# Performance work log

Hardware: AMD Instinct MI355X
Metric: run time of the kernel (lower is better)

## Reference

```python
import jax, jax.numpy as jnp
import numpy as np

T, B, D_IN, D_H = 1024, 64, 256, 256


def setup_inputs() -> dict:
    key = jax.random.key(0)
    ks = jax.random.split(key, 9)
    s = 1.0 / np.sqrt(D_IN + D_H)  # torch Linear default init scale
    def lin(k):
        kw, kb = jax.random.split(k)
        W = jax.random.uniform(kw, (D_H, D_IN + D_H), minval=-s, maxval=s, dtype=jnp.float32)
        b = jax.random.uniform(kb, (D_H,), minval=-s, maxval=s, dtype=jnp.float32)
        return W, b
    W_f, b_f = lin(ks[0])
    W_i, b_i = lin(ks[1])
    W_g, b_g = lin(ks[2])
    W_o, b_o = lin(ks[3])
    inputs = jax.random.normal(ks[4], (T, B, D_IN), dtype=jnp.float32)
    h0 = jnp.zeros((B, D_H), dtype=jnp.float32)
    c0 = jnp.zeros((B, D_H), dtype=jnp.float32)
    return {"inputs": inputs, "h0": h0, "c0": c0,
            "W_f": W_f, "b_f": b_f, "W_i": W_i, "b_i": b_i,
            "W_g": W_g, "b_g": b_g, "W_o": W_o, "b_o": b_o}


def reference(inputs, h0, c0, W_f, b_f, W_i, b_i, W_g, b_g, W_o, b_o):
    # Fuse the 4 gate GEMMs into one: stack weights -> [4H, D_in+H]
    W = jnp.concatenate([W_f, W_i, W_g, W_o], axis=0)      # [4H, D]
    b = jnp.concatenate([b_f, b_i, b_g, b_o], axis=0)      # [4H]
    H = h0.shape[-1]

    def step(carry, x):
        h, c = carry
        combined = jnp.concatenate([x, h], axis=1)          # [B, D_in+H]
        gates = combined @ W.T + b                          # [B, 4H]
        f = jax.nn.sigmoid(gates[:, 0 * H:1 * H])
        i = jax.nn.sigmoid(gates[:, 1 * H:2 * H])
        g = jnp.tanh(gates[:, 2 * H:3 * H])
        o = jax.nn.sigmoid(gates[:, 3 * H:4 * H])
        c_new = f * c + i * g
        h_new = o * jnp.tanh(c_new)
        return (h_new, c_new), h_new

    (h, c), outputs = jax.lax.scan(step, (h0, c0), inputs)
    return outputs, h, c
```

## Files before the change

kernel.cpp:

```cpp
#include <hip/hip_runtime.h>
#include <cstdint>
#include <cstddef>

#define T_STEPS 1024
#define NB 64
#define DIN 256
#define DH 256
#define DW 512
#define G4 1024

typedef _Float16 h2 __attribute__((ext_vector_type(2)));
typedef _Float16 h4 __attribute__((ext_vector_type(4)));
typedef _Float16 h8 __attribute__((ext_vector_type(8)));
typedef float f4 __attribute__((ext_vector_type(4)));
typedef float f32x4 __attribute__((ext_vector_type(4)));
typedef int i4v __attribute__((ext_vector_type(4)));

static __device__ __forceinline__ float rcp_(float x) {
#if __has_builtin(__builtin_amdgcn_rcpf)
  return __builtin_amdgcn_rcpf(x);
#else
  return 1.0f / x;
#endif
}

static __device__ __forceinline__ float sigmoid_(float x) {
  return rcp_(1.f + __expf(-x));
}
static __device__ __forceinline__ float tanh_(float x) {
  float e = __expf(2.f * x);
  return 1.f - 2.f * rcp_(e + 1.f);
}

static __device__ __forceinline__ int sdot4_(int a, int b, int c) {
#if __has_builtin(__builtin_amdgcn_sdot4)
  return __builtin_amdgcn_sdot4(a, b, c, false);
#else
  int r = c;
#pragma unroll
  for (int k = 0; k < 4; ++k)
    r += (int)(signed char)(a >> (8 * k)) * (int)(signed char)(b >> (8 * k));
  return r;
#endif
}

static __device__ __forceinline__ float dpp_swap1(float x) {
  int r = __builtin_amdgcn_update_dpp(0, __builtin_bit_cast(int, x),
                                      0xB1, 0xF, 0xF, true);
  return __builtin_bit_cast(float, r);
}

__global__ void kconv_w(const float* __restrict__ Wf, const float* __restrict__ Wi,
                        const float* __restrict__ Wg, const float* __restrict__ Wo,
                        h2* __restrict__ wxfs) {
  int kp = blockIdx.x >> 2;
  int gate = blockIdx.x & 3;
  int j = threadIdx.x;
  const float* W = gate == 0 ? Wf : gate == 1 ? Wi : gate == 2 ? Wg : Wo;
  const float* row = W + (size_t)j * DW;
  h2 v; v[0] = (_Float16)row[2*kp]; v[1] = (_Float16)row[2*kp + 1];
  int ks = kp >> 4, lg = (kp >> 2) & 3, slot = kp & 3;
  int nt = j >> 4, li = j & 15;
  size_t h8idx = (((size_t)gate * 8 + ks) * 16 + nt) * 64 + lg * 16 + li;
  wxfs[h8idx * 4 + slot] = v;
}

__global__ void kscale(const float* __restrict__ Wf, const float* __restrict__ Wi,
                       const float* __restrict__ Wg, const float* __restrict__ Wo,
                       signed char* __restrict__ wq, float* __restrict__ cs) {
  int gate = blockIdx.x;
  int j = threadIdx.x;
  const float* W = gate == 0 ? Wf : gate == 1 ? Wi : gate == 2 ? Wg : Wo;
  const float* row = W + (size_t)j * DW + DIN;
  float amax = 1e-8f;
#pragma unroll 4
  for (int k4 = 0; k4 < 64; ++k4) {
    f4 v = *(const f4*)(row + 4 * k4);
    amax = fmaxf(amax, fmaxf(fmaxf(fabsf(v[0]), fabsf(v[1])),
                             fmaxf(fabsf(v[2]), fabsf(v[3]))));
  }
  int gr = gate * 256 + j;
  cs[gr] = amax / (127.f * 127.f);
  float inv = 127.f / amax;
  signed char* dst = wq + (size_t)gr * 256;
#pragma unroll 4
  for (int k4 = 0; k4 < 64; ++k4) {
    f4 v = *(const f4*)(row + 4 * k4);
#pragma unroll
    for (int u = 0; u < 4; ++u)
      dst[4 * k4 + u] = (signed char)__float2int_rn(v[u] * inv);
  }
}

__launch_bounds__(256, 2)
__global__ void kxgemm(const float* __restrict__ x,
                       const h8* __restrict__ wxfs,
                       const float* __restrict__ bf, const float* __restrict__ bi,
                       const float* __restrict__ bg, const float* __restrict__ bo,
                       _Float16* __restrict__ Xg,
                       int t0) {
  __shared__ char pool[65536];
  h8 (*xsf)[8][64] = (h8(*)[8][64])pool;
  h8 (*bs)[1024] = (h8(*)[1024])(pool + 32768);

  int tid = threadIdx.x;
  int l = tid & 63;
  int w = tid >> 6;
  int li = l & 15, lg = l >> 4;
  int tl = blockIdx.x >> 2;
  int nb = blockIdx.x & 3;
  int m0 = w * 16;

#pragma unroll
  for (int i = 0; i < 8; ++i) {
    int hi = tid + 256 * i;
    int sw  = hi >> 9;
    int sks = (hi >> 6) & 7;
    int sl  = hi & 63;
    int sli = sl & 15, slg = sl >> 4;
    const float* src = x + ((size_t)(t0 + tl) * NB + sw * 16 + sli) * DIN
                     + sks * 32 + slg * 8;
    f4 a0 = *(const f4*)src;
    f4 a1 = *(const f4*)(src + 4);
    h8 a;
    a[0] = (_Float16)a0[0]; a[1] = (_Float16)a0[1];
    a[2] = (_Float16)a0[2]; a[3] = (_Float16)a0[3];
    a[4] = (_Float16)a1[0]; a[5] = (_Float16)a1[1];
    a[6] = (_Float16)a1[2]; a[7] = (_Float16)a1[3];
    xsf[sw][sks][sl] = a;
  }
  {
    const h8* wsrc = wxfs + (size_t)(nb * 8 + 0) * 1024;
#pragma unroll
    for (int i = 0; i < 4; ++i) bs[0][tid + 256 * i] = wsrc[tid + 256 * i];
  }
  __syncthreads();

  f32x4 acc[16];
#pragma unroll
  for (int nt = 0; nt < 16; ++nt) {
    acc[nt][0] = 0.f; acc[nt][1] = 0.f; acc[nt][2] = 0.f; acc[nt][3] = 0.f;
  }

  for (int ks = 0; ks < 8; ++ks) {
    int buf = ks & 1;
    h8 ld0, ld1, ld2, ld3;
    if (ks < 7) {
      const h8* wn = wxfs + (size_t)(nb * 8 + ks + 1) * 1024;
      ld0 = wn[tid]; ld1 = wn[tid + 256]; ld2 = wn[tid + 512]; ld3 = wn[tid + 768];
    }
    h8 a = xsf[w][ks][l];
#pragma unroll
    for (int nt = 0; nt < 16; ++nt) {
      h8 bb = bs[buf][nt * 64 + l];
      acc[nt] = __builtin_amdgcn_mfma_f32_16x16x32_f16(a, bb, acc[nt], 0, 0, 0);
    }
    if (ks < 7) {
      h8* bt = bs[buf ^ 1];
      bt[tid] = ld0; bt[tid + 256] = ld1; bt[tid + 512] = ld2; bt[tid + 768] = ld3;
    }
    __syncthreads();
  }

  _Float16* osw = (_Float16*)(pool + (size_t)w * 8448);
  const float* biasp = nb == 0 ? bf : nb == 1 ? bi : nb == 2 ? bg : bo;
#pragma unroll
  for (int nt = 0; nt < 16; ++nt) {
    float bv = biasp[nt * 16 + li];
#pragma unroll
    for (int r = 0; r < 4; ++r)
      osw[(lg * 4 + r) * 264 + nt * 16 + li] = (_Float16)(acc[nt][r] + bv);
  }
  _Float16* og = Xg + (size_t)tl * 65536 + (size_t)m0 * 1024 + nb * 256;
#pragma unroll
  for (int it = 0; it < 8; ++it) {
    int i = l + 64 * it;
    int row = i >> 5, c8 = i & 31;
    h8 v = *(const h8*)(const void*)&osw[row * 264 + c8 * 8];
    *(h8*)(void*)(og + (size_t)row * 1024 + c8 * 8) = v;
  }
}

#define CH8(M) M(0) M(1) M(2) M(3) M(4) M(5) M(6) M(7)
#define HB 144

__global__ __launch_bounds__(512, 1)
void klstm(const signed char* __restrict__ wq, const float* __restrict__ cs,
           const _Float16* __restrict__ Xg,
           const float* __restrict__ hsrc, const float* __restrict__ csrc,
           float* __restrict__ out,
           float* __restrict__ hN, float* __restrict__ cN,
           int t0, int Tc) {
  __shared__ __align__(16) char hpool[2][43008];

  int tid = threadIdx.x;
  int b = blockIdx.x;
  int p = tid & 1;
  int j = tid >> 1;

  const i4v* rF = (const i4v*)(wq + ((size_t)(0 * DH + j) * 256) + p * 128);
  const i4v* rI = (const i4v*)(wq + ((size_t)(1 * DH + j) * 256) + p * 128);
  const i4v* rG = (const i4v*)(wq + ((size_t)(2 * DH + j) * 256) + p * 128);
  const i4v* rO = (const i4v*)(wq + ((size_t)(3 * DH + j) * 256) + p * 128);

#define DECLW(c) i4v QF_##c, QI_##c, QG_##c, QO_##c;
  CH8(DECLW)
#undef DECLW
#define LOADW(c) \
  QF_##c = rF[c]; QI_##c = rI[c]; QG_##c = rG[c]; QO_##c = rO[c];
  CH8(LOADW)
#undef LOADW
#define PINW(c) \
  asm volatile("" : "+v"(QF_##c)); asm volatile("" : "+v"(QI_##c)); \
  asm volatile("" : "+v"(QG_##c)); asm volatile("" : "+v"(QO_##c));
  CH8(PINW)
#undef PINW

  float cF = cs[0 * DH + j];
  float cI = cs[1 * DH + j];
  float cG = cs[2 * DH + j];
  float cO = cs[3 * DH + j];

  float creg = csrc[(size_t)b * DH + j];
  if (tid < 256) {
    int pos = (tid < 128) ? tid : (HB + tid - 128);
    float hv = hsrc[(size_t)b * DH + tid];
    hpool[0][pos] = (char)__float2int_rn(fminf(fmaxf(hv, -1.f), 1.f) * 127.f);
  }
  __syncthreads();

  const size_t xstep = (size_t)NB * G4;
  const _Float16* xpA = Xg + (size_t)b * G4 + p * 512 + j;
  const _Float16* xpB = xpA + 256;
  float xA = (float)xpA[0], xB = (float)xpB[0];
  float hlast = 0.f;

  for (int t = 0; t < Tc; ++t) {
    float xAn = 0.f, xBn = 0.f;
    if (t + 1 < Tc) {
      xAn = (float)xpA[(size_t)(t + 1) * xstep];
      xBn = (float)xpB[(size_t)(t + 1) * xstep];
    }
    const char* hb = hpool[t & 1] + p * HB;

    int aF = 0, aI = 0, aG = 0, aO = 0;
#define DOTC(c) { \
    i4v hv = *(const i4v*)(const void*)(hb + 16 * (c)); \
    aF = sdot4_(QF_##c[0], hv[0], aF); aF = sdot4_(QF_##c[1], hv[1], aF); \
    aF = sdot4_(QF_##c[2], hv[2], aF); aF = sdot4_(QF_##c[3], hv[3], aF); \
    aI = sdot4_(QI_##c[0], hv[0], aI); aI = sdot4_(QI_##c[1], hv[1], aI); \
    aI = sdot4_(QI_##c[2], hv[2], aI); aI = sdot4_(QI_##c[3], hv[3], aI); \
    aG = sdot4_(QG_##c[0], hv[0], aG); aG = sdot4_(QG_##c[1], hv[1], aG); \
    aG = sdot4_(QG_##c[2], hv[2], aG); aG = sdot4_(QG_##c[3], hv[3], aG); \
    aO = sdot4_(QO_##c[0], hv[0], aO); aO = sdot4_(QO_##c[1], hv[1], aO); \
    aO = sdot4_(QO_##c[2], hv[2], aO); aO = sdot4_(QO_##c[3], hv[3], aO); }
    CH8(DOTC)
#undef DOTC

    float vF = cF * (float)aF + (p ? 0.f : xA);
    float vI = cI * (float)aI + (p ? 0.f : xB);
    float vG = cG * (float)aG + (p ? xA : 0.f);
    float vO = cO * (float)aO + (p ? xB : 0.f);
    vF += dpp_swap1(vF);
    vI += dpp_swap1(vI);
    vG += dpp_swap1(vG);
    vO += dpp_swap1(vO);

    float f_ = sigmoid_(vF);
    float i_ = sigmoid_(vI);
    float g_ = tanh_(vG);
    float o_ = sigmoid_(vO);

    creg = f_ * creg + i_ * g_;
    float hn = o_ * tanh_(creg);
    hlast = hn;
    if (p == 0) {
      out[((size_t)(t0 + t) * NB + b) * DH + j] = hn;
    } else {
      int pos = (j < 128) ? j : (HB + j - 128);
      hpool[(t + 1) & 1][pos] = (char)__float2int_rn(hn * 127.f);
    }
    __syncthreads();
    xA = xAn; xB = xBn;
  }

  if (p == 0) {
    hN[(size_t)b * DH + j] = hlast;
    cN[(size_t)b * DH + j] = creg;
  }
}

extern "C" void kernel_launch(void* const* d_in, const int* in_sizes, int n_in,
                              void* d_out, int out_size, void* d_ws, size_t ws_size,
                              hipStream_t stream) {
  if (n_in < 11) return;
  const float* x  = (const float*)d_in[0];
  const float* h0 = (const float*)d_in[1];
  const float* c0 = (const float*)d_in[2];
  const float* Wf = (const float*)d_in[3];
  const float* bf = (const float*)d_in[4];
  const float* Wi = (const float*)d_in[5];
  const float* bi = (const float*)d_in[6];
  const float* Wg = (const float*)d_in[7];
  const float* bg = (const float*)d_in[8];
  const float* Wo = (const float*)d_in[9];
  const float* bo = (const float*)d_in[10];

  float* out = (float*)d_out;
  float* hN = out + (size_t)T_STEPS * NB * DH;
  float* cN = hN + (size_t)NB * DH;

  const size_t wxfBytes = (size_t)G4 * 128 * sizeof(h2);
  const size_t wqBytes  = (size_t)G4 * 256;
  const size_t csBytes  = (size_t)G4 * sizeof(float);
  const size_t fixedBytes = wxfBytes + wqBytes + csBytes;
  size_t avail = (ws_size > fixedBytes + 512) ? ws_size - fixedBytes - 512 : 0;
  const size_t perT = (size_t)NB * G4 * 2;
  int Tc = (int)(avail / perT);
  if (Tc > T_STEPS) Tc = T_STEPS;
  if (Tc < 1) Tc = 1;

  _Float16* Xg = (_Float16*)d_ws;
  size_t xgBytes = ((size_t)Tc * perT + 255) / 256 * 256;
  h2* wxfs = (h2*)((char*)d_ws + xgBytes);
  signed char* wq = (signed char*)((char*)d_ws + xgBytes + wxfBytes);
  float* cs = (float*)((char*)d_ws + xgBytes + wxfBytes + wqBytes);

  kconv_w<<<dim3(512), dim3(256), 0, stream>>>(Wf, Wi, Wg, Wo, wxfs);
  kscale<<<dim3(4), dim3(256), 0, stream>>>(Wf, Wi, Wg, Wo, wq, cs);

  for (int t0 = 0; t0 < T_STEPS; t0 += Tc) {
    int tc = (T_STEPS - t0 < Tc) ? (T_STEPS - t0) : Tc;
    kxgemm<<<dim3(tc * 4), dim3(256), 0, stream>>>(x, (const h8*)wxfs,
                                                   bf, bi, bg, bo, Xg, t0);
    const float* hs = (t0 == 0) ? h0 : hN;
    const float* cs_ = (t0 == 0) ? c0 : cN;
    klstm<<<dim3(NB), dim3(512), 0, stream>>>(wq, cs, Xg, hs, cs_,
                                              out, hN, cN, t0, tc);
  }
}
```

Measured before the change: 1.244 ms.

## Process two batch rows per block in LSTM recurrence, halving grid size

Each klstm block now handles two batch elements, reusing the register-resident int8 weights for both hidden vectors and interleaving the two dot-product chains for more ILP. The grid drops from 64 to 32 blocks, and the shared-memory buffer shrinks from a large pool to a small double buffer. Output stores are deferred by one step so they overlap with the next step's compute. Fewer blocks means fewer CUs in use and about twice the per-step work in each block, which could lengthen the serial critical path.

```diff
diff --git a/kernel.cpp b/kernel.cpp
--- a/kernel.cpp
+++ b/kernel.cpp
@@ -183,6 +183,7 @@
 
 #define CH8(M) M(0) M(1) M(2) M(3) M(4) M(5) M(6) M(7)
 #define HB 144
+#define BB 288
 
 __global__ __launch_bounds__(512, 1)
 void klstm(const signed char* __restrict__ wq, const float* __restrict__ cs,
@@ -191,10 +192,11 @@
            float* __restrict__ out,
            float* __restrict__ hN, float* __restrict__ cN,
            int t0, int Tc) {
-  __shared__ __align__(16) char hpool[2][43008];
+  __shared__ __align__(16) char hp[2][2 * BB];
 
   int tid = threadIdx.x;
-  int b = blockIdx.x;
+  int b0 = blockIdx.x * 2;
+  int b1 = b0 + 1;
   int p = tid & 1;
   int j = tid >> 1;
 
@@ -221,72 +223,109 @@
   float cG = cs[2 * DH + j];
   float cO = cs[3 * DH + j];
 
-  float creg = csrc[(size_t)b * DH + j];
-  if (tid < 256) {
-    int pos = (tid < 128) ? tid : (HB + tid - 128);
-    float hv = hsrc[(size_t)b * DH + tid];
-    hpool[0][pos] = (char)__float2int_rn(fminf(fmaxf(hv, -1.f), 1.f) * 127.f);
+  float creg0 = csrc[(size_t)b0 * DH + j];
+  float creg1 = csrc[(size_t)b1 * DH + j];
+
+  {
+    int bt = tid >> 8, e = tid & 255;
+    int pos = (e < 128) ? e : (HB + e - 128);
+    float hv = hsrc[(size_t)(b0 + bt) * DH + e];
+    hp[0][bt * BB + pos] = (char)__float2int_rn(fminf(fmaxf(hv, -1.f), 1.f) * 127.f);
   }
   __syncthreads();
 
   const size_t xstep = (size_t)NB * G4;
-  const _Float16* xpA = Xg + (size_t)b * G4 + p * 512 + j;
-  const _Float16* xpB = xpA + 256;
-  float xA = (float)xpA[0], xB = (float)xpB[0];
-  float hlast = 0.f;
+  const _Float16* xA0p = Xg + (size_t)b0 * G4 + p * 512 + j;
+  const _Float16* xB0p = xA0p + 256;
+  const _Float16* xA1p = Xg + (size_t)b1 * G4 + p * 512 + j;
+  const _Float16* xB1p = xA1p + 256;
+  float xA0 = (float)xA0p[0], xB0 = (float)xB0p[0];
+  float xA1 = (float)xA1p[0], xB1 = (float)xB1p[0];
+  float hp0 = 0.f, hp1 = 0.f;
+  float hl0 = 0.f, hl1 = 0.f;
+
+  float* ob0 = out + (size_t)b0 * DH + j;
+  float* ob1 = out + (size_t)b1 * DH + j;
 
   for (int t = 0; t < Tc; ++t) {
-    float xAn = 0.f, xBn = 0.f;
+    if (p == 0 && t > 0) {
+      ob0[(size_t)(t0 + t - 1) * NB * DH] = hp0;
+      ob1[(size_t)(t0 + t - 1) * NB * DH] = hp1;
+    }
+    float xA0n = 0.f, xB0n = 0.f, xA1n = 0.f, xB1n = 0.f;
     if (t + 1 < Tc) {
-      xAn = (float)xpA[(size_t)(t + 1) * xstep];
-      xBn = (float)xpB[(size_t)(t + 1) * xstep];
-    }
-    const char* hb = hpool[t & 1] + p * HB;
-
-    int aF = 0, aI = 0, aG = 0, aO = 0;
+      size_t o = (size_t)(t + 1) * xstep;
+      xA0n = (float)xA0p[o]; xB0n = (float)xB0p[o];
+      xA1n = (float)xA1p[o]; xB1n = (float)xB1p[o];
+    }
+    const char* hbA = hp[t & 1] + p * HB;
+    const char* hbB = hp[t & 1] + BB + p * HB;
+
+    int aF0 = 0, aI0 = 0, aG0 = 0, aO0 = 0;
+    int aF1 = 0, aI1 = 0, aG1 = 0, aO1 = 0;
 #define DOTC(c) { \
-    i4v hv = *(const i4v*)(const void*)(hb + 16 * (c)); \
-    aF = sdot4_(QF_##c[0], hv[0], aF); aF = sdot4_(QF_##c[1], hv[1], aF); \
-    aF = sdot4_(QF_##c[2], hv[2], aF); aF = sdot4_(QF_##c[3], hv[3], aF); \
-    aI = sdot4_(QI_##c[0], hv[0], aI); aI = sdot4_(QI_##c[1], hv[1], aI); \
-    aI = sdot4_(QI_##c[2], hv[2], aI); aI = sdot4_(QI_##c[3], hv[3], aI); \
-    aG = sdot4_(QG_##c[0], hv[0], aG); aG = sdot4_(QG_##c[1], hv[1], aG); \
-    aG = sdot4_(QG_##c[2], hv[2], aG); aG = sdot4_(QG_##c[3], hv[3], aG); \
-    aO = sdot4_(QO_##c[0], hv[0], aO); aO = sdot4_(QO_##c[1], hv[1], aO); \
-    aO = sdot4_(QO_##c[2], hv[2], aO); aO = sdot4_(QO_##c[3], hv[3], aO); }
+    i4v hA = *(const i4v*)(const void*)(hbA + 16 * (c)); \
+    i4v hB = *(const i4v*)(const void*)(hbB + 16 * (c)); \
+    aF0 = sdot4_(QF_##c[0], hA[0], aF0); aF1 = sdot4_(QF_##c[0], hB[0], aF1); \
+    aF0 = sdot4_(QF_##c[1], hA[1], aF0); aF1 = sdot4_(QF_##c[1], hB[1], aF1); \
+    aF0 = sdot4_(QF_##c[2], hA[2], aF0); aF1 = sdot4_(QF_##c[2], hB[2], aF1); \
+    aF0 = sdot4_(QF_##c[3], hA[3], aF0); aF1 = sdot4_(QF_##c[3], hB[3], aF1); \
+    aI0 = sdot4_(QI_##c[0], hA[0], aI0); aI1 = sdot4_(QI_##c[0], hB[0], aI1); \
+    aI0 = sdot4_(QI_##c[1], hA[1], aI0); aI1 = sdot4_(QI_##c[1], hB[1], aI1); \
+    aI0 = sdot4_(QI_##c[2], hA[2], aI0); aI1 = sdot4_(QI_##c[2], hB[2], aI1); \
+    aI0 = sdot4_(QI_##c[3], hA[3], aI0); aI1 = sdot4_(QI_##c[3], hB[3], aI1); \
+    aG0 = sdot4_(QG_##c[0], hA[0], aG0); aG1 = sdot4_(QG_##c[0], hB[0], aG1); \
+    aG0 = sdot4_(QG_##c[1], hA[1], aG0); aG1 = sdot4_(QG_##c[1], hB[1], aG1); \
+    aG0 = sdot4_(QG_##c[2], hA[2], aG0); aG1 = sdot4_(QG_##c[2], hB[2], aG1); \
+    aG0 = sdot4_(QG_##c[3], hA[3], aG0); aG1 = sdot4_(QG_##c[3], hB[3], aG1); \
+    aO0 = sdot4_(QO_##c[0], hA[0], aO0); aO1 = sdot4_(QO_##c[0], hB[0], aO1); \
+    aO0 = sdot4_(QO_##c[1], hA[1], aO0); aO1 = sdot4_(QO_##c[1], hB[1], aO1); \
+    aO0 = sdot4_(QO_##c[2], hA[2], aO0); aO1 = sdot4_(QO_##c[2], hB[2], aO1); \
+    aO0 = sdot4_(QO_##c[3], hA[3], aO0); aO1 = sdot4_(QO_##c[3], hB[3], aO1); }
     CH8(DOTC)
 #undef DOTC
 
-    float vF = cF * (float)aF + (p ? 0.f : xA);
-    float vI = cI * (float)aI + (p ? 0.f : xB);
-    float vG = cG * (float)aG + (p ? xA : 0.f);
-    float vO = cO * (float)aO + (p ? xB : 0.f);
-    vF += dpp_swap1(vF);
-    vI += dpp_swap1(vI);
-    vG += dpp_swap1(vG);
-    vO += dpp_swap1(vO);
-
-    float f_ = sigmoid_(vF);
-    float i_ = sigmoid_(vI);
-    float g_ = tanh_(vG);
-    float o_ = sigmoid_(vO);
-
-    creg = f_ * creg + i_ * g_;
-    float hn = o_ * tanh_(creg);
-    hlast = hn;
-    if (p == 0) {
-      out[((size_t)(t0 + t) * NB + b) * DH + j] = hn;
-    } else {
+    float vF0 = cF * (float)aF0 + (p ? 0.f : xA0);
+    float vI0 = cI * (float)aI0 + (p ? 0.f : xB0);
+    float vG0 = cG * (float)aG0 + (p ? xA0 : 0.f);
+    float vO0 = cO * (float)aO0 + (p ? xB0 : 0.f);
+    float vF1 = cF * (float)aF1 + (p ? 0.f : xA1);
+    float vI1 = cI * (float)aI1 + (p ? 0.f : xB1);
+    float vG1 = cG * (float)aG1 + (p ? xA1 : 0.f);
+    float vO1 = cO * (float)aO1 + (p ? xB1 : 0.f);
+    vF0 += dpp_swap1(vF0); vF1 += dpp_swap1(vF1);
+    vI0 += dpp_swap1(vI0); vI1 += dpp_swap1(vI1);
+    vG0 += dpp_swap1(vG0); vG1 += dpp_swap1(vG1);
+    vO0 += dpp_swap1(vO0); vO1 += dpp_swap1(vO1);
+
+    float f0 = sigmoid_(vF0), f1 = sigmoid_(vF1);
+    float i0 = sigmoid_(vI0), i1 = sigmoid_(vI1);
+    float g0 = tanh_(vG0),    g1 = tanh_(vG1);
+    float o0 = sigmoid_(vO0), o1 = sigmoid_(vO1);
+
+    creg0 = f0 * creg0 + i0 * g0;
+    creg1 = f1 * creg1 + i1 * g1;
+    float hn0 = o0 * tanh_(creg0);
+    float hn1 = o1 * tanh_(creg1);
+    hl0 = hn0; hl1 = hn1;
+    hp0 = hn0; hp1 = hn1;
+    if (p == 1) {
       int pos = (j < 128) ? j : (HB + j - 128);
-      hpool[(t + 1) & 1][pos] = (char)__float2int_rn(hn * 127.f);
+      char* dst = hp[(t + 1) & 1];
+      dst[pos]      = (char)__float2int_rn(hn0 * 127.f);
+      dst[BB + pos] = (char)__float2int_rn(hn1 * 127.f);
     }
     __syncthreads();
-    xA = xAn; xB = xBn;
+    xA0 = xA0n; xB0 = xB0n; xA1 = xA1n; xB1 = xB1n;
   }
 
   if (p == 0) {
-    hN[(size_t)b * DH + j] = hlast;
-    cN[(size_t)b * DH + j] = creg;
+    ob0[(size_t)(t0 + Tc - 1) * NB * DH] = hp0;
+    ob1[(size_t)(t0 + Tc - 1) * NB * DH] = hp1;
+    hN[(size_t)b0 * DH + j] = hl0;
+    hN[(size_t)b1 * DH + j] = hl1;
+    cN[(size_t)b0 * DH + j] = creg0;
+    cN[(size_t)b1 * DH + j] = creg1;
   }
 }
 
@@ -335,7 +374,7 @@
                                                    bf, bi, bg, bo, Xg, t0);
     const float* hs = (t0 == 0) ? h0 : hN;
     const float* cs_ = (t0 == 0) ? c0 : cN;
-    klstm<<<dim3(NB), dim3(512), 0, stream>>>(wq, cs, Xg, hs, cs_,
-                                              out, hN, cN, t0, tc);
-  }
-}
+    klstm<<<dim3(NB / 2), dim3(512), 0, stream>>>(wq, cs, Xg, hs, cs_,
+                                                  out, hN, cN, t0, tc);
+  }
+}
```

New measurement: 2.020 ms. 1.62x slower.
